# Kernel tuning notes

Hardware: AMD Instinct MI355X
Metric: run time of the kernel (lower is better)

Reference implementation:

```python
import jax, jax.numpy as jnp
import numpy as np

N, C_A, C_S, C_Z, H = 1024, 768, 384, 128, 16
D = C_A // H  # 48


def _ln(x, gamma=None, beta=None, eps=1e-5):
    m = jnp.mean(x, axis=-1, keepdims=True)
    v = jnp.var(x, axis=-1, keepdims=True)
    y = (x - m) * jax.lax.rsqrt(v + eps)
    if gamma is not None:
        y = y * gamma
    if beta is not None:
        y = y + beta
    return y


def _adaln(a, s, gamma_s, Wg, bg, Wadd):
    # AF3 Algorithm 26: LN(a) w/o affine, LN(s) w/ scale only; gate + additive shift from s
    a_ln = _ln(a)
    s_ln = _ln(s, gamma_s)
    return jax.nn.sigmoid(s_ln @ Wg + bg) * a_ln + s_ln @ Wadd


def setup_inputs() -> dict:
    key = jax.random.key(0)
    ks = iter(jax.random.split(key, 40))
    def nrm(shape, scale=0.02):
        return jax.random.normal(next(ks), shape, dtype=jnp.float32) * scale
    f32 = jnp.float32
    return dict(
        a=jax.random.normal(next(ks), (1, N, C_A), dtype=f32),
        s=jax.random.normal(next(ks), (1, N, C_S), dtype=f32),
        z=jax.random.normal(next(ks), (1, N, N, C_Z), dtype=f32),
        # AdaptiveLayerNorm (attention branch)
        gamma_s1=jnp.ones((C_S,), f32), Wg1=nrm((C_S, C_A)), bg1=jnp.zeros((C_A,), f32), Wadd1=nrm((C_S, C_A)),
        # pair-bias: LN(z) scale-only + LinearNoBias(c_z -> n_heads)
        gamma_z=jnp.ones((C_Z,), f32), Wz=nrm((C_Z, H)),
        # Attention: q has bias, k/v no bias, sigmoid gating, output proj
        Wq=nrm((C_A, C_A)), bq=jnp.zeros((C_A,), f32),
        Wk=nrm((C_A, C_A)), Wv=nrm((C_A, C_A)),
        Wgate=nrm((C_A, C_A)), bgate=jnp.ones((C_A,), f32),
        Wo=nrm((C_A, C_A)), bo=jnp.zeros((C_A,), f32),
        # BiasInitLinear output gate (biasinit=-2)
        Ws_last=nrm((C_S, C_A)), bs_last=jnp.full((C_A,), -2.0, f32),
        # ConditionedTransitionBlock (n=2)
        gamma_s2=jnp.ones((C_S,), f32), Wg2=nrm((C_S, C_A)), bg2=jnp.zeros((C_A,), f32), Wadd2=nrm((C_S, C_A)),
        W1=nrm((C_A, 2 * C_A)), W2=nrm((C_A, 2 * C_A)), Wb=nrm((2 * C_A, C_A)),
        Ws_t=nrm((C_S, C_A)), b_t=jnp.full((C_A,), -2.0, f32),
    )


def reference(a, s, z, gamma_s1, Wg1, bg1, Wadd1, gamma_z, Wz,
              Wq, bq, Wk, Wv, Wgate, bgate, Wo, bo, Ws_last, bs_last,
              gamma_s2, Wg2, bg2, Wadd2, W1, W2, Wb, Ws_t, b_t):
    B = a.shape[0]
    # ---- AttentionPairBias (standard / global path) ----
    a_ln = _adaln(a, s, gamma_s1, Wg1, bg1, Wadd1)
    bias = _ln(z, gamma_z) @ Wz                     # [B, N, N, H]
    bias = jnp.moveaxis(bias, -1, -3)               # [B, H, N, N]
    q = (a_ln @ Wq + bq).reshape(B, N, H, D)
    k = (a_ln @ Wk).reshape(B, N, H, D)
    v = (a_ln @ Wv).reshape(B, N, H, D)
    scale = 1.0 / float(np.sqrt(D))
    scores = jnp.einsum('bqhd,bkhd->bhqk', q, k) * scale + bias
    attn = jax.nn.softmax(scores, axis=-1)
    o = jnp.einsum('bhqk,bkhd->bqhd', attn, v)      # [B, N, H, D]
    g = jax.nn.sigmoid(a_ln @ Wgate + bgate).reshape(B, N, H, D)
    o = (g * o).reshape(B, N, C_A) @ Wo + bo
    attn_out = jax.nn.sigmoid(s @ Ws_last + bs_last) * o
    # ---- ConditionedTransitionBlock (Algorithm 25, n=2) ----
    a2 = _adaln(a, s, gamma_s2, Wg2, bg2, Wadd2)
    bmid = jax.nn.silu(a2 @ W1) * (a2 @ W2)
    t_out = jax.nn.sigmoid(s @ Ws_t + b_t) * (bmid @ Wb)
    # Algorithm 23 line 2-3: a = b + ConditionedTransitionBlock(a, s)
    return attn_out + t_out
```

## Files before the change

kernel.cpp:

```cpp
#include <hip/hip_runtime.h>

typedef __bf16 bf16;
typedef __bf16 v8bf __attribute__((ext_vector_type(8)));
typedef float  v4f  __attribute__((ext_vector_type(4)));
typedef short  short4v __attribute__((ext_vector_type(4)));

__device__ __forceinline__ float sigf(float x){ return 1.0f/(1.0f + __expf(-x)); }

typedef __attribute__((address_space(3))) unsigned int lds_u32;
typedef __attribute__((address_space(1))) const unsigned int gbl_u32;
__device__ __forceinline__ void gl16(const void* g, void* l) {
  __builtin_amdgcn_global_load_lds((gbl_u32*)g, (lds_u32*)l, 16, 0, 0);
}

struct WTab {
  const float* src[14];
  bf16* dst[14];
  int K[14], N[14], boff[14];
};

__global__ __launch_bounds__(256) void k_prepw(WTab tab) {
  __shared__ float lds[32][33];
  int bid = blockIdx.x;
  int e = 0;
  #pragma unroll
  for (int i = 1; i < 14; i++) if (tab.boff[i] <= bid) e = i;
  int local = bid - tab.boff[e];
  int K = tab.K[e], N = tab.N[e];
  int nKT = K >> 5;
  int kt = local % nKT, nt = local / nKT;
  int k0 = kt * 32, n0 = nt * 32;
  const float* src = tab.src[e];
  bf16* dst = tab.dst[e];
  int tx = threadIdx.x & 31, ty = threadIdx.x >> 5;
  #pragma unroll
  for (int i = 0; i < 4; i++)
    lds[ty + i*8][tx] = src[(long)(k0 + ty + i*8) * N + n0 + tx];
  __syncthreads();
  #pragma unroll
  for (int i = 0; i < 4; i++)
    dst[(long)(n0 + ty + i*8) * K + k0 + tx] = (bf16)lds[tx][ty + i*8];
}

__global__ void k_prepz(const float* __restrict__ Wz, const float* __restrict__ gz,
                        bf16* __restrict__ wzT) {
  int t = blockIdx.x * 256 + threadIdx.x;
  int k = t >> 4, h = t & 15;
  wzT[h * 128 + k] = (bf16)(Wz[t] * gz[k]);
}

__global__ __launch_bounds__(256) void k_ln_a(const float* __restrict__ a,
                                              float* __restrict__ out) {
  int row = blockIdx.x;
  const float* x = a + (long)row * 768;
  int t = threadIdx.x;
  float lv[3], s = 0.f, q = 0.f;
  #pragma unroll
  for (int i = 0; i < 3; i++){ lv[i] = x[t + i*256]; s += lv[i]; q += lv[i]*lv[i]; }
  #pragma unroll
  for (int m = 1; m < 64; m <<= 1){ s += __shfl_xor(s, m); q += __shfl_xor(q, m); }
  __shared__ float ls[4], lq[4];
  int w = t >> 6, lane = t & 63;
  if (!lane){ ls[w] = s; lq[w] = q; }
  __syncthreads();
  s = ls[0]+ls[1]+ls[2]+ls[3]; q = lq[0]+lq[1]+lq[2]+lq[3];
  float mean = s * (1.f/768.f);
  float var  = q * (1.f/768.f) - mean*mean;
  float inv  = rsqrtf(var + 1e-5f);
  float* o = out + (long)row * 768;
  #pragma unroll
  for (int i = 0; i < 3; i++) o[t + i*256] = (lv[i] - mean) * inv;
}

__global__ __launch_bounds__(128) void k_ln_s(const float* __restrict__ sIn,
    const float* __restrict__ g1, const float* __restrict__ g2,
    bf16* __restrict__ s1, bf16* __restrict__ s2, bf16* __restrict__ sb) {
  int row = blockIdx.x;
  const float* x = sIn + (long)row * 384;
  int t = threadIdx.x;
  float lv[3], s = 0.f, q = 0.f;
  #pragma unroll
  for (int i = 0; i < 3; i++){ lv[i] = x[t + i*128]; s += lv[i]; q += lv[i]*lv[i]; }
  #pragma unroll
  for (int m = 1; m < 64; m <<= 1){ s += __shfl_xor(s, m); q += __shfl_xor(q, m); }
  __shared__ float ls[2], lq[2];
  int w = t >> 6, lane = t & 63;
  if (!lane){ ls[w] = s; lq[w] = q; }
  __syncthreads();
  s = ls[0] + ls[1]; q = lq[0] + lq[1];
  float mean = s * (1.f/384.f);
  float var  = q * (1.f/384.f) - mean*mean;
  float inv  = rsqrtf(var + 1e-5f);
  long base = (long)row * 384;
  #pragma unroll
  for (int i = 0; i < 3; i++){
    int c = t + i*128;
    float y = (lv[i] - mean) * inv;
    s1[base + c] = (bf16)(y * g1[c]);
    s2[base + c] = (bf16)(y * g2[c]);
    sb[base + c] = (bf16)lv[i];
  }
}

__device__ __forceinline__ void zbias_body(int bid, char* smem,
    const float* __restrict__ z, const bf16* __restrict__ wzT,
    bf16* __restrict__ biasb) {
  float (*pb)[17] = (float(*)[17])smem;
  int t = threadIdx.x, lane = t & 63, w = t >> 6;
  int r16 = lane & 15, g4 = lane >> 4;
  long base = (long)bid * 64;
  long pos = base + w*16 + r16;
  const float* zr = z + pos * 128;
  float4 xv[8];
  #pragma unroll
  for (int s = 0; s < 4; s++) {
    xv[2*s]   = *reinterpret_cast<const float4*>(&zr[s*32 + g4*8]);
    xv[2*s+1] = *reinterpret_cast<const float4*>(&zr[s*32 + g4*8 + 4]);
  }
  const float* x = reinterpret_cast<const float*>(xv);
  float sm = 0.f, q = 0.f;
  #pragma unroll
  for (int i = 0; i < 32; i++){ sm += x[i]; q += x[i]*x[i]; }
  sm += __shfl_xor(sm, 16); q += __shfl_xor(q, 16);
  sm += __shfl_xor(sm, 32); q += __shfl_xor(q, 32);
  float mean = sm * (1.f/128.f), var = q * (1.f/128.f) - mean*mean;
  float inv = rsqrtf(var + 1e-5f);
  v4f acc = (v4f){0.f, 0.f, 0.f, 0.f};
  #pragma unroll
  for (int s = 0; s < 4; s++) {
    union { bf16 b[8]; v8bf v; } ua;
    #pragma unroll
    for (int j = 0; j < 8; j++) ua.b[j] = (bf16)((x[s*8 + j] - mean) * inv);
    v8bf bw = *reinterpret_cast<const v8bf*>(&wzT[r16*128 + s*32 + g4*8]);
    acc = __builtin_amdgcn_mfma_f32_16x16x32_bf16(ua.v, bw, acc, 0, 0, 0);
  }
  #pragma unroll
  for (int r = 0; r < 4; r++) pb[w*16 + g4*4 + r][r16] = acc[r];
  __syncthreads();
  int p = t & 63, hb = t >> 6;
  #pragma unroll
  for (int j = 0; j < 4; j++) {
    int h = hb*4 + j;
    biasb[((long)h << 20) + base + p] = (bf16)pb[p][h];
  }
}

#define EPI_ADASG  0
#define EPI_SWIGLU 1
#define EPI_QKVG   2
#define EPI_WO     6
#define EPI_WB     7

template<int TM, int TN, bool DUAL, int EPI>
__device__ __forceinline__ void gemm_body(
    bf16* As, bf16* Bs, int m0, int n0, int z,
    const bf16* __restrict__ Ap, const bf16* __restrict__ B1, long sBpair, int K,
    const float* __restrict__ f0, const float* __restrict__ f1,
    const float* __restrict__ f2, const float* __restrict__ f3,
    const float* __restrict__ f4, const bf16* __restrict__ bb0,
    void* __restrict__ outp, long sOutz)
{
  constexpr int WM = TM/2, WN = TN/2;
  constexpr int MI = WM/16, NI = WN/16;
  const bf16* B2 = B1 + sBpair;
  int t = threadIdx.x, lane = t & 63, w = t >> 6;
  int wr = w >> 1, wc = w & 1;
  int r16 = lane & 15, g4 = lane >> 4;
  constexpr int NACC = DUAL ? 2 : 1;
  v4f acc[NACC][MI][NI];
  #pragma unroll
  for (int d = 0; d < NACC; d++)
    #pragma unroll
    for (int mi = 0; mi < MI; mi++)
      #pragma unroll
      for (int ni = 0; ni < NI; ni++)
        acc[d][mi][ni] = (v4f){0.f, 0.f, 0.f, 0.f};

  for (int k0 = 0; k0 < K; k0 += 64) {
    #pragma unroll
    for (int cb = 0; cb < TM/32; cb++) {
      int cc = cb*4 + w;
      int c16 = cc*64 + lane;
      int row = c16 >> 3, col = c16 & 7;
      int scol = col ^ (row & 7);
      gl16(&Ap[(long)(m0 + row)*K + k0 + scol*8], (char*)As + cc*1024);
    }
    #pragma unroll
    for (int cb = 0; cb < TN/32; cb++) {
      int cc = cb*4 + w;
      int c16 = cc*64 + lane;
      int row = c16 >> 3, col = c16 & 7;
      int scol = col ^ (row & 7);
      gl16(&B1[(long)(n0 + row)*K + k0 + scol*8], (char*)Bs + cc*1024);
      if constexpr (DUAL)
        gl16(&B2[(long)(n0 + row)*K + k0 + scol*8], (char*)Bs + TN*128 + cc*1024);
    }
    __syncthreads();
    #pragma unroll
    for (int s = 0; s < 2; s++) {
      int ch = s*4 + g4;
      v8bf af[MI];
      #pragma unroll
      for (int mi = 0; mi < MI; mi++) {
        int ra = wr*WM + mi*16 + r16;
        af[mi] = *reinterpret_cast<const v8bf*>(
            (const char*)As + ra*128 + ((ch ^ (ra & 7)) << 4));
      }
      #pragma unroll
      for (int d = 0; d < NACC; d++)
        #pragma unroll
        for (int ni = 0; ni < NI; ni++) {
          int rb = wc*WN + ni*16 + r16;
          v8bf bfv = *reinterpret_cast<const v8bf*>(
              (const char*)Bs + d*(TN*128) + rb*128 + ((ch ^ (rb & 7)) << 4));
          #pragma unroll
          for (int mi = 0; mi < MI; mi++)
            acc[d][mi][ni] = __builtin_amdgcn_mfma_f32_16x16x32_bf16(af[mi], bfv, acc[d][mi][ni], 0, 0, 0);
        }
    }
    __syncthreads();
  }

  int colb = n0 + wc*WN + r16;
  int rowb = m0 + wr*WM + (g4 << 2);
  #pragma unroll
  for (int mi = 0; mi < MI; mi++)
    #pragma unroll
    for (int ni = 0; ni < NI; ni++) {
      int col = colb + ni*16;
      if constexpr (EPI == EPI_ADASG) {
        if (z < 2) {
          float bg = (z == 0 ? f1 : f2)[col];
          bf16* o = (bf16*)outp + (long)z * sOutz;
          #pragma unroll
          for (int r = 0; r < 4; r++) {
            long idx = (long)(rowb + mi*16 + r)*768 + col;
            float gl = acc[0][mi][ni][r] + bg;
            o[idx] = (bf16)(sigf(gl) * f0[idx] + acc[1][mi][ni][r]);
          }
        } else {
          bf16* o0 = (bf16*)outp + 2*sOutz;
          bf16* o1 = (bf16*)outp + 3*sOutz;
          #pragma unroll
          for (int r = 0; r < 4; r++) {
            long idx = (long)(rowb + mi*16 + r)*768 + col;
            o0[idx] = (bf16)sigf(acc[0][mi][ni][r] + f3[col]);
            o1[idx] = (bf16)sigf(acc[1][mi][ni][r] + f4[col]);
          }
        }
      } else if constexpr (EPI == EPI_SWIGLU) {
        bf16* o = (bf16*)outp;
        #pragma unroll
        for (int r = 0; r < 4; r++) {
          long idx = (long)(rowb + mi*16 + r)*1536 + col;
          float x1 = acc[0][mi][ni][r], x2 = acc[1][mi][ni][r];
          o[idx] = (bf16)(x1 * sigf(x1) * x2);
        }
      } else if constexpr (EPI == EPI_QKVG) {
        int h = col / 48, d = col - h*48;
        if (z == 0) {
          const float qs = 0.14433756729740643f;
          bf16* qp = (bf16*)outp;
          #pragma unroll
          for (int r = 0; r < 4; r++)
            qp[(long)h*65536 + (long)(rowb + mi*16 + r)*64 + d] =
              (bf16)((acc[0][mi][ni][r] + f0[col]) * qs);
        } else if (z == 1) {
          bf16* kp = (bf16*)outp + sOutz;
          #pragma unroll
          for (int r = 0; r < 4; r++)
            kp[(long)h*65536 + (long)(rowb + mi*16 + r)*64 + d] = (bf16)acc[0][mi][ni][r];
        } else if (z == 2) {
          bf16* vT = (bf16*)outp + 2*sOutz;
          union { bf16 h4[4]; short4v s4; } u;
          #pragma unroll
          for (int r = 0; r < 4; r++) u.h4[r] = (bf16)acc[0][mi][ni][r];
          *reinterpret_cast<short4v*>(&vT[(long)h*65536 + (long)d*1024 + rowb + mi*16]) = u.s4;
        } else {
          bf16* gp = (bf16*)outp + 3*sOutz;
          #pragma unroll
          for (int r = 0; r < 4; r++)
            gp[(long)(rowb + mi*16 + r)*768 + col] = (bf16)sigf(acc[0][mi][ni][r] + f1[col]);
        }
      } else if constexpr (EPI == EPI_WO) {
        float* o = (float*)outp;
        #pragma unroll
        for (int r = 0; r < 4; r++) {
          long idx = (long)(rowb + mi*16 + r)*768 + col;
          o[idx] = (float)bb0[idx] * (acc[0][mi][ni][r] + f0[col]);
        }
      } else {
        float* o = (float*)outp;
        #pragma unroll
        for (int r = 0; r < 4; r++) {
          long idx = (long)(rowb + mi*16 + r)*768 + col;
          o[idx] = f0[idx] + (float)bb0[idx] * acc[0][mi][ni][r];
        }
      }
    }
}

template<int TM, int TN, bool DUAL, int EPI>
__global__ __launch_bounds__(256) void gemm_k(
    const bf16* A, const bf16* B, long sAz, long sBz, long sBpair, int K,
    const float* f0, const float* f1, const float* f2, const float* f3,
    const float* f4, const bf16* bb0, void* outp, long sOutz)
{
  __shared__ __align__(16) bf16 As[TM*64];
  __shared__ __align__(16) bf16 Bs[(DUAL?2:1)*TN*64];
  int z = blockIdx.z;
  gemm_body<TM,TN,DUAL,EPI>(As, Bs, blockIdx.y*TM, blockIdx.x*TN, z,
      A + (long)z*sAz, B + (long)z*sBz, sBpair, K,
      f0, f1, f2, f3, f4, bb0, outp, sOutz);
}

__global__ __launch_bounds__(256, 4) void k_mega(
    const bf16* aln, const bf16* wQKVG, const float* bq, const float* bgate,
    bf16* qkv, const bf16* a2b, const bf16* wW12, bf16* bmid,
    const float* Zin, const bf16* wzT, bf16* biasb)
{
  __shared__ __align__(16) char smem[24576];
  int bid = blockIdx.x;
  if (bid < 768) {
    int z = bid / 192, rem = bid % 192;
    gemm_body<64,64,false,EPI_QKVG>((bf16*)smem, (bf16*)(smem + 8192),
        (rem/12)*64, (rem%12)*64, z,
        aln, wQKVG + (long)z*589824, 0, 768,
        bq, bgate, nullptr, nullptr, nullptr, nullptr, qkv, 1048576);
  } else if (bid < 1152) {
    int rem = bid - 768;
    gemm_body<64,64,true,EPI_SWIGLU>((bf16*)smem, (bf16*)(smem + 8192),
        (rem/24)*64, (rem%24)*64, 0,
        a2b, wW12, 1179648, 768,
        nullptr, nullptr, nullptr, nullptr, nullptr, nullptr, bmid, 0);
  } else {
    zbias_body(bid - 1152, smem, Zin, wzT, biasb);
  }
}

__global__ __launch_bounds__(256) void k_flash(
    const bf16* __restrict__ qp, const bf16* __restrict__ kp,
    const bf16* __restrict__ vT, const bf16* __restrict__ biasb,
    const bf16* __restrict__ gp, bf16* __restrict__ gob)
{
  __shared__ bf16 pl[4][16*72];
  int t = threadIdx.x, lane = t & 63, w = t >> 6;
  int h = blockIdx.y;
  int q0 = blockIdx.x * 64 + w * 16;
  int r16 = lane & 15, g4 = lane >> 4;
  const bf16* qb = qp + ((long)h << 16);
  const bf16* kb = kp + ((long)h << 16);
  const bf16* vb = vT + ((long)h << 16);
  const bf16* bb = biasb + ((long)h << 20) + (long)q0 * 1024;

  v8bf qa[2];
  #pragma unroll
  for (int s = 0; s < 2; s++)
    qa[s] = *reinterpret_cast<const v8bf*>(&qb[(long)(q0 + r16)*64 + s*32 + g4*8]);

  v4f oacc[4];
  #pragma unroll
  for (int nd = 0; nd < 4; nd++) oacc[nd] = (v4f){0.f, 0.f, 0.f, 0.f};
  float mrun[4], lrun[4];
  #pragma unroll
  for (int r = 0; r < 4; r++){ mrun[r] = -1e30f; lrun[r] = 0.f; }

  for (int kt = 0; kt < 16; kt++) {
    int k0 = kt * 64;
    v4f sacc[4];
    #pragma unroll
    for (int nk = 0; nk < 4; nk++) sacc[nk] = (v4f){0.f, 0.f, 0.f, 0.f};
    #pragma unroll
    for (int nk = 0; nk < 4; nk++)
      #pragma unroll
      for (int s = 0; s < 2; s++) {
        v8bf kf = *reinterpret_cast<const v8bf*>(&kb[(long)(k0 + nk*16 + r16)*64 + s*32 + g4*8]);
        sacc[nk] = __builtin_amdgcn_mfma_f32_16x16x32_bf16(qa[s], kf, sacc[nk], 0, 0, 0);
      }
    float mtile[4];
    #pragma unroll
    for (int r = 0; r < 4; r++) mtile[r] = -1e30f;
    #pragma unroll
    for (int nk = 0; nk < 4; nk++)
      #pragma unroll
      for (int r = 0; r < 4; r++) {
        float bvv = (float)bb[(long)(g4*4 + r)*1024 + k0 + nk*16 + r16];
        sacc[nk][r] += bvv;
        mtile[r] = fmaxf(mtile[r], sacc[nk][r]);
      }
    #pragma unroll
    for (int r = 0; r < 4; r++) {
      #pragma unroll
      for (int m = 1; m < 16; m <<= 1) mtile[r] = fmaxf(mtile[r], __shfl_xor(mtile[r], m));
    }
    float scl[4], rsum[4];
    #pragma unroll
    for (int r = 0; r < 4; r++) {
      float mn = fmaxf(mrun[r], mtile[r]);
      scl[r] = __expf(mrun[r] - mn);
      mrun[r] = mn;
      rsum[r] = 0.f;
    }
    bf16* plw = &pl[w][0];
    #pragma unroll
    for (int nk = 0; nk < 4; nk++)
      #pragma unroll
      for (int r = 0; r < 4; r++) {
        float p = __expf(sacc[nk][r] - mrun[r]);
        rsum[r] += p;
        plw[(g4*4 + r)*72 + nk*16 + r16] = (bf16)p;
      }
    #pragma unroll
    for (int r = 0; r < 4; r++) {
      #pragma unroll
      for (int m = 1; m < 16; m <<= 1) rsum[r] += __shfl_xor(rsum[r], m);
      lrun[r] = lrun[r]*scl[r] + rsum[r];
      #pragma unroll
      for (int nd = 0; nd < 4; nd++) oacc[nd][r] *= scl[r];
    }
    v8bf pa[2];
    #pragma unroll
    for (int s = 0; s < 2; s++)
      pa[s] = *reinterpret_cast<const v8bf*>(&plw[r16*72 + s*32 + g4*8]);
    #pragma unroll
    for (int nd = 0; nd < 4; nd++)
      #pragma unroll
      for (int s = 0; s < 2; s++) {
        v8bf vf = *reinterpret_cast<const v8bf*>(&vb[(long)(nd*16 + r16)*1024 + k0 + s*32 + g4*8]);
        oacc[nd] = __builtin_amdgcn_mfma_f32_16x16x32_bf16(pa[s], vf, oacc[nd], 0, 0, 0);
      }
  }
  #pragma unroll
  for (int r = 0; r < 4; r++) {
    int qrow = q0 + g4*4 + r;
    float invl = 1.0f / lrun[r];
    #pragma unroll
    for (int nd = 0; nd < 3; nd++) {
      long idx = (long)qrow*768 + h*48 + nd*16 + r16;
      gob[idx] = (bf16)(oacc[nd][r] * invl * (float)gp[idx]);
    }
  }
}

extern "C" void kernel_launch(void* const* d_in, const int* in_sizes, int n_in,
                              void* d_out, int out_size, void* d_ws, size_t ws_size,
                              hipStream_t stream)
{
  const float* A_in  = (const float*)d_in[0];
  const float* S_in  = (const float*)d_in[1];
  const float* Z_in  = (const float*)d_in[2];
  const float* g_s1  = (const float*)d_in[3];
  const float* Wg1   = (const float*)d_in[4];
  const float* bg1   = (const float*)d_in[5];
  const float* Wadd1 = (const float*)d_in[6];
  const float* g_z   = (const float*)d_in[7];
  const float* Wz    = (const float*)d_in[8];
  const float* Wq    = (const float*)d_in[9];
  const float* bq    = (const float*)d_in[10];
  const float* Wk    = (const float*)d_in[11];
  const float* Wv    = (const float*)d_in[12];
  const float* Wgate = (const float*)d_in[13];
  const float* bgate = (const float*)d_in[14];
  const float* Wo    = (const float*)d_in[15];
  const float* bo    = (const float*)d_in[16];
  const float* WsL   = (const float*)d_in[17];
  const float* bsL   = (const float*)d_in[18];
  const float* g_s2  = (const float*)d_in[19];
  const float* Wg2   = (const float*)d_in[20];
  const float* bg2   = (const float*)d_in[21];
  const float* Wadd2 = (const float*)d_in[22];
  const float* W1    = (const float*)d_in[23];
  const float* W2    = (const float*)d_in[24];
  const float* Wb    = (const float*)d_in[25];
  const float* WsT   = (const float*)d_in[26];
  const float* b_t   = (const float*)d_in[27];
  float* OUT = (float*)d_out;

  char* ws = (char*)d_ws;
  size_t off = 0;
  auto alloc = [&](size_t bytes) -> void* {
    void* p = ws + off; off += (bytes + 255) & ~(size_t)255; return p; };

  bf16*  wGA6  = (bf16*) alloc(6ul*294912*2);
  bf16*  wQKVG = (bf16*) alloc(4ul*589824*2);
  bf16*  wWoT  = (bf16*) alloc(589824ul*2);
  bf16*  wW12  = (bf16*) alloc(2ul*1179648*2);
  bf16*  wWbT  = (bf16*) alloc(1179648ul*2);
  bf16*  wzT   = (bf16*) alloc(2048ul*2);
  bf16*  sl1   = (bf16*) alloc(393216ul*2);
  bf16*  sl2   = (bf16*) alloc(393216ul*2);
  bf16*  sbf   = (bf16*) alloc(393216ul*2);
  float* alnr  = (float*)alloc(786432ul*4);
  bf16*  aln   = (bf16*) alloc(786432ul*2);
  bf16*  a2b   = (bf16*) alloc(786432ul*2);
  bf16*  sgf   = (bf16*) alloc(2ul*786432*2);
  bf16*  qkv   = (bf16*) alloc((3ul*1048576 + 786432)*2);
  bf16*  biasb = (bf16*) alloc(16777216ul*2);
  bf16*  gob   = (bf16*) alloc(786432ul*2);
  float* opj   = (float*)alloc(786432ul*4);
  bf16*  bmid  = (bf16*) alloc(1572864ul*2);

  WTab tab;
  auto setw = [&](int i, const float* src, bf16* dst, int K, int N){
    tab.src[i] = src; tab.dst[i] = dst; tab.K[i] = K; tab.N[i] = N; };
  setw(0,  Wg1,   wGA6,             384,  768);
  setw(1,  Wadd1, wGA6 + 294912,    384,  768);
  setw(2,  Wg2,   wGA6 + 589824,    384,  768);
  setw(3,  Wadd2, wGA6 + 884736,    384,  768);
  setw(4,  WsL,   wGA6 + 1179648,   384,  768);
  setw(5,  WsT,   wGA6 + 1474560,   384,  768);
  setw(6,  Wq,    wQKVG,            768,  768);
  setw(7,  Wk,    wQKVG + 589824,   768,  768);
  setw(8,  Wv,    wQKVG + 2*589824, 768,  768);
  setw(9,  Wgate, wQKVG + 3*589824, 768,  768);
  setw(10, Wo,    wWoT,             768,  768);
  setw(11, W1,    wW12,             768, 1536);
  setw(12, W2,    wW12 + 1179648,   768, 1536);
  setw(13, Wb,    wWbT,            1536,  768);
  int boff = 0;
  for (int i = 0; i < 14; i++){ tab.boff[i] = boff; boff += (tab.K[i]/32)*(tab.N[i]/32); }

  k_prepw<<<boff, 256, 0, stream>>>(tab);
  k_prepz<<<8, 256, 0, stream>>>(Wz, g_z, wzT);
  k_ln_a<<<1024, 256, 0, stream>>>(A_in, alnr);
  k_ln_s<<<1024, 128, 0, stream>>>(S_in, g_s1, g_s2, sl1, sl2, sbf);
  (void)hipMemsetAsync(qkv, 0, 3ul*1048576*2, stream);

  gemm_k<64,64,true,EPI_ADASG><<<dim3(12,16,3), 256, 0, stream>>>(
      sl1, wGA6, 393216, 589824, 294912, 384,
      alnr, bg1, bg2, bsL, b_t, nullptr, aln, 786432);

  k_mega<<<17536, 256, 0, stream>>>(
      aln, wQKVG, bq, bgate, qkv, a2b, wW12, bmid, Z_in, wzT, biasb);

  k_flash<<<dim3(16,16), 256, 0, stream>>>(
      qkv, qkv + 1048576, qkv + 2097152, biasb, qkv + 3145728, gob);

  gemm_k<64,64,false,EPI_WO><<<dim3(12,16,1), 256, 0, stream>>>(
      gob, wWoT, 0, 0, 0, 768,
      bo, nullptr, nullptr, nullptr, nullptr, sgf, opj, 0);

  gemm_k<64,64,false,EPI_WB><<<dim3(12,16,1), 256, 0, stream>>>(
      bmid, wWbT, 0, 0, 0, 1536,
      opj, nullptr, nullptr, nullptr, nullptr, sgf + 786432, OUT, 0);
}
```

Baseline: 241.9 us.

## Merge prep kernels and co-schedule Wb GEMM with flash attention

Four small prep kernels (weight transpose, Wz prep, LN of a, LN of s) become one launch, with blocks dispatched by index range and two s rows handled per 256-thread block. The Wb transition GEMM now runs in the same launch as flash attention, writing its gated result straight to the output. The Wo GEMM then adds its gated result into that output, so the opj intermediate buffer and its extra read and write go away. This saves launch overhead and lets the independent Wb GEMM fill idle CUs while the 256-block attention runs, but the shared-memory size of the combined kernel may lower occupancy for the flash blocks.

Result: slower. 272.8 us (+12.8%).

```diff
diff --git a/kernel.cpp b/kernel.cpp
--- a/kernel.cpp
+++ b/kernel.cpp
@@ -19,9 +19,8 @@
   int K[14], N[14], boff[14];
 };
 
-__global__ __launch_bounds__(256) void k_prepw(WTab tab) {
-  __shared__ float lds[32][33];
-  int bid = blockIdx.x;
+__device__ __forceinline__ void prepw_body(int bid, char* smem, const WTab& tab) {
+  float (*lds)[33] = (float(*)[33])smem;
   int e = 0;
   #pragma unroll
   for (int i = 1; i < 14; i++) if (tab.boff[i] <= bid) e = i;
@@ -42,16 +41,8 @@
     dst[(long)(n0 + ty + i*8) * K + k0 + tx] = (bf16)lds[tx][ty + i*8];
 }
 
-__global__ void k_prepz(const float* __restrict__ Wz, const float* __restrict__ gz,
-                        bf16* __restrict__ wzT) {
-  int t = blockIdx.x * 256 + threadIdx.x;
-  int k = t >> 4, h = t & 15;
-  wzT[h * 128 + k] = (bf16)(Wz[t] * gz[k]);
-}
-
-__global__ __launch_bounds__(256) void k_ln_a(const float* __restrict__ a,
-                                              float* __restrict__ out) {
-  int row = blockIdx.x;
+__device__ __forceinline__ void ln_a_body(int row, const float* __restrict__ a,
+                                          float* __restrict__ out) {
   const float* x = a + (long)row * 768;
   int t = threadIdx.x;
   float lv[3], s = 0.f, q = 0.f;
@@ -72,26 +63,27 @@
   for (int i = 0; i < 3; i++) o[t + i*256] = (lv[i] - mean) * inv;
 }
 
-__global__ __launch_bounds__(128) void k_ln_s(const float* __restrict__ sIn,
+__device__ __forceinline__ void ln_s_body(int row, const float* __restrict__ sIn,
     const float* __restrict__ g1, const float* __restrict__ g2,
     bf16* __restrict__ s1, bf16* __restrict__ s2, bf16* __restrict__ sb) {
-  int row = blockIdx.x;
-  const float* x = sIn + (long)row * 384;
-  int t = threadIdx.x;
+  int t = threadIdx.x & 127;
+  int sub = threadIdx.x >> 7;
+  int r = row*2 + sub;
+  const float* x = sIn + (long)r * 384;
   float lv[3], s = 0.f, q = 0.f;
   #pragma unroll
   for (int i = 0; i < 3; i++){ lv[i] = x[t + i*128]; s += lv[i]; q += lv[i]*lv[i]; }
   #pragma unroll
   for (int m = 1; m < 64; m <<= 1){ s += __shfl_xor(s, m); q += __shfl_xor(q, m); }
-  __shared__ float ls[2], lq[2];
-  int w = t >> 6, lane = t & 63;
-  if (!lane){ ls[w] = s; lq[w] = q; }
+  __shared__ float ls[2][2], lq[2][2];
+  int w = (t >> 6) & 1, lane = t & 63;
+  if (!lane){ ls[sub][w] = s; lq[sub][w] = q; }
   __syncthreads();
-  s = ls[0] + ls[1]; q = lq[0] + lq[1];
+  s = ls[sub][0] + ls[sub][1]; q = lq[sub][0] + lq[sub][1];
   float mean = s * (1.f/384.f);
   float var  = q * (1.f/384.f) - mean*mean;
   float inv  = rsqrtf(var + 1e-5f);
-  long base = (long)row * 384;
+  long base = (long)r * 384;
   #pragma unroll
   for (int i = 0; i < 3; i++){
     int c = t + i*128;
@@ -100,6 +92,28 @@
     s2[base + c] = (bf16)(y * g2[c]);
     sb[base + c] = (bf16)lv[i];
   }
+}
+
+__global__ __launch_bounds__(256) void k_prep(WTab tab, int boffTot,
+    const float* Wz, const float* gz, bf16* wzT,
+    const float* A_in, float* alnr,
+    const float* S_in, const float* g1, const float* g2,
+    bf16* sl1, bf16* sl2, bf16* sbf)
+{
+  __shared__ __align__(16) char smem[4224];
+  int bid = blockIdx.x;
+  if (bid < boffTot) { prepw_body(bid, smem, tab); return; }
+  bid -= boffTot;
+  if (bid < 8) {
+    int t = bid * 256 + threadIdx.x;
+    int k = t >> 4, h = t & 15;
+    wzT[h * 128 + k] = (bf16)(Wz[t] * gz[k]);
+    return;
+  }
+  bid -= 8;
+  if (bid < 1024) { ln_a_body(bid, A_in, alnr); return; }
+  bid -= 1024;
+  ln_s_body(bid, S_in, g1, g2, sl1, sl2, sbf);
 }
 
 __device__ __forceinline__ void zbias_body(int bid, char* smem,
@@ -287,14 +301,14 @@
         #pragma unroll
         for (int r = 0; r < 4; r++) {
           long idx = (long)(rowb + mi*16 + r)*768 + col;
-          o[idx] = (float)bb0[idx] * (acc[0][mi][ni][r] + f0[col]);
+          o[idx] = o[idx] + (float)bb0[idx] * (acc[0][mi][ni][r] + f0[col]);
         }
       } else {
         float* o = (float*)outp;
         #pragma unroll
         for (int r = 0; r < 4; r++) {
           long idx = (long)(rowb + mi*16 + r)*768 + col;
-          o[idx] = f0[idx] + (float)bb0[idx] * acc[0][mi][ni][r];
+          o[idx] = (float)bb0[idx] * acc[0][mi][ni][r];
         }
       }
     }
@@ -338,16 +352,15 @@
   }
 }
 
-__global__ __launch_bounds__(256) void k_flash(
+__device__ __forceinline__ void flash_body(int qt, int h, char* smem,
     const bf16* __restrict__ qp, const bf16* __restrict__ kp,
     const bf16* __restrict__ vT, const bf16* __restrict__ biasb,
     const bf16* __restrict__ gp, bf16* __restrict__ gob)
 {
-  __shared__ bf16 pl[4][16*72];
   int t = threadIdx.x, lane = t & 63, w = t >> 6;
-  int h = blockIdx.y;
-  int q0 = blockIdx.x * 64 + w * 16;
+  int q0 = qt * 64 + w * 16;
   int r16 = lane & 15, g4 = lane >> 4;
+  bf16* plw = (bf16*)smem + w * 1152;
   const bf16* qb = qp + ((long)h << 16);
   const bf16* kb = kp + ((long)h << 16);
   const bf16* vb = vT + ((long)h << 16);
@@ -401,7 +414,6 @@
       mrun[r] = mn;
       rsum[r] = 0.f;
     }
-    bf16* plw = &pl[w][0];
     #pragma unroll
     for (int nk = 0; nk < 4; nk++)
       #pragma unroll
@@ -439,6 +451,24 @@
       long idx = (long)qrow*768 + h*48 + nd*16 + r16;
       gob[idx] = (bf16)(oacc[nd][r] * invl * (float)gp[idx]);
     }
+  }
+}
+
+__global__ __launch_bounds__(256) void k_tail(
+    const bf16* bmid, const bf16* wWbT, const bf16* sgf1, float* OUT,
+    const bf16* qp, const bf16* kp, const bf16* vT, const bf16* biasb,
+    const bf16* gp, bf16* gob)
+{
+  __shared__ __align__(16) char smem[16384];
+  int bid = blockIdx.x;
+  if (bid < 192) {
+    gemm_body<64,64,false,EPI_WB>((bf16*)smem, (bf16*)(smem + 8192),
+        (bid/12)*64, (bid%12)*64, 0,
+        bmid, wWbT, 0, 1536,
+        nullptr, nullptr, nullptr, nullptr, nullptr, sgf1, OUT, 0);
+  } else {
+    int local = bid - 192;
+    flash_body(local & 15, local >> 4, smem, qp, kp, vT, biasb, gp, gob);
   }
 }
 
@@ -497,7 +527,6 @@
   bf16*  qkv   = (bf16*) alloc((3ul*1048576 + 786432)*2);
   bf16*  biasb = (bf16*) alloc(16777216ul*2);
   bf16*  gob   = (bf16*) alloc(786432ul*2);
-  float* opj   = (float*)alloc(786432ul*4);
   bf16*  bmid  = (bf16*) alloc(1572864ul*2);
 
   WTab tab;
@@ -520,11 +549,10 @@
   int boff = 0;
   for (int i = 0; i < 14; i++){ tab.boff[i] = boff; boff += (tab.K[i]/32)*(tab.N[i]/32); }
 
-  k_prepw<<<boff, 256, 0, stream>>>(tab);
-  k_prepz<<<8, 256, 0, stream>>>(Wz, g_z, wzT);
-  k_ln_a<<<1024, 256, 0, stream>>>(A_in, alnr);
-  k_ln_s<<<1024, 128, 0, stream>>>(S_in, g_s1, g_s2, sl1, sl2, sbf);
   (void)hipMemsetAsync(qkv, 0, 3ul*1048576*2, stream);
+
+  k_prep<<<boff + 8 + 1024 + 512, 256, 0, stream>>>(
+      tab, boff, Wz, g_z, wzT, A_in, alnr, S_in, g_s1, g_s2, sl1, sl2, sbf);
 
   gemm_k<64,64,true,EPI_ADASG><<<dim3(12,16,3), 256, 0, stream>>>(
       sl1, wGA6, 393216, 589824, 294912, 384,
@@ -533,14 +561,11 @@
   k_mega<<<17536, 256, 0, stream>>>(
       aln, wQKVG, bq, bgate, qkv, a2b, wW12, bmid, Z_in, wzT, biasb);
 
-  k_flash<<<dim3(16,16), 256, 0, stream>>>(
+  k_tail<<<448, 256, 0, stream>>>(
+      bmid, wWbT, sgf + 786432, OUT,
       qkv, qkv + 1048576, qkv + 2097152, biasb, qkv + 3145728, gob);
 
   gemm_k<64,64,false,EPI_WO><<<dim3(12,16,1), 256, 0, stream>>>(
       gob, wWoT, 0, 0, 0, 768,
-      bo, nullptr, nullptr, nullptr, nullptr, sgf, opj, 0);
-
-  gemm_k<64,64,false,EPI_WB><<<dim3(12,16,1), 256, 0, stream>>>(
-      bmid, wWbT, 0, 0, 0, 1536,
-      opj, nullptr, nullptr, nullptr, nullptr, sgf + 786432, OUT, 0);
-}
+      bo, nullptr, nullptr, nullptr, nullptr, sgf, OUT, 0);
+}
```
